# Optimization experiments

Measured on AMD Instinct MI355X. Metric: run time of the kernel, lower is better.

Reference implementation:

```python
import jax, jax.numpy as jnp
import numpy as np

STEPS = 10
HIDDEN = 16


def _lift_world(uv, depth, cam2world, intrinsics):
    # uv: [B,N,2], depth: [B,N], returns world coords [B,N,3]
    fx = intrinsics[:, 0, 0][:, None]
    fy = intrinsics[:, 1, 1][:, None]
    cx = intrinsics[:, 0, 2][:, None]
    cy = intrinsics[:, 1, 2][:, None]
    x_lift = (uv[:, :, 0] - cx) / fx * depth
    y_lift = (uv[:, :, 1] - cy) / fy * depth
    pts_hom = jnp.stack((x_lift, y_lift, depth, jnp.ones_like(depth)), axis=-1)  # [B,N,4]
    world = jnp.einsum('bij,bnj->bni', cam2world, pts_hom)[:, :, :3]
    return world


def reference(cam2world, intrinsics, uv, initial_depth,
              W_phi, b_phi, W_ih, b_ih, W_hh, b_hh, W_out, b_out):
    B, N, _ = uv.shape
    F = W_phi.shape[1]

    # ray directions through pixels (z_cam = 1 plane)
    pixel_pts = _lift_world(uv, jnp.ones((B, N), uv.dtype), cam2world, intrinsics)
    cam_pos = cam2world[:, :3, 3]
    ray_dirs = pixel_pts - cam_pos[:, None, :]
    ray_dirs = ray_dirs / jnp.linalg.norm(ray_dirs, axis=2, keepdims=True)

    world0 = _lift_world(uv, initial_depth[:, :, 0], cam2world, intrinsics)

    h0 = jnp.zeros((B * N, HIDDEN), world0.dtype)
    c0 = jnp.zeros((B * N, HIDDEN), world0.dtype)

    def step(carry, _):
        world, h, c = carry
        # phi: per-point feature net (stand-in: relu(Linear 3->F))
        v = jax.nn.relu(jnp.einsum('bnd,df->bnf', world, W_phi) + b_phi)
        x = v.reshape(B * N, F)
        gates = x @ W_ih.T + b_ih + h @ W_hh.T + b_hh  # [BN, 4H]
        i, f, g, o = jnp.split(gates, 4, axis=1)  # torch LSTMCell gate order
        c = jax.nn.sigmoid(f) * c + jax.nn.sigmoid(i) * jnp.tanh(g)
        h = jax.nn.sigmoid(o) * jnp.tanh(c)
        sd = (h @ W_out.T + b_out).reshape(B, N, 1)  # signed distance
        world = world + ray_dirs * sd
        return (world, h, c), None

    (world, _, _), _ = jax.lax.scan(step, (world0, h0, c0), None, length=STEPS)

    # final depth: camera-frame z of world points
    pts_hom = jnp.concatenate((world, jnp.ones((B, N, 1), world.dtype)), axis=2)
    c2w_inv = jnp.linalg.inv(cam2world)
    pts_cam = jnp.einsum('bij,bnj->bni', c2w_inv, pts_hom)
    depth = pts_cam[:, :, 2:3]
    return world, depth


def setup_inputs() -> dict:
    key = jax.random.key(0)
    ks = jax.random.split(key, 12)
    B, N, F = 8, 16384, 256
    H = HIDDEN

    # cam2world: proper-ish poses (orthonormal rotation via QR + translation)
    R = jnp.linalg.qr(jax.random.normal(ks[0], (B, 3, 3)))[0]
    t = jax.random.normal(ks[1], (B, 3)) * 2.0
    cam2world = jnp.zeros((B, 4, 4)).at[:, :3, :3].set(R).at[:, :3, 3].set(t).at[:, 3, 3].set(1.0)

    intrinsics = jnp.zeros((B, 3, 3))
    intrinsics = intrinsics.at[:, 0, 0].set(500.0).at[:, 1, 1].set(500.0)
    intrinsics = intrinsics.at[:, 0, 2].set(64.0).at[:, 1, 2].set(64.0).at[:, 2, 2].set(1.0)

    uv = jax.random.uniform(ks[2], (B, N, 2)) * 128.0  # pixel coords in a 128x128 image
    initial_depth = 0.05 + 0.0005 * jax.random.normal(ks[3], (B, N, 1))

    s = 1.0 / np.sqrt(F)
    return {
        'cam2world': cam2world.astype(jnp.float32),
        'intrinsics': intrinsics.astype(jnp.float32),
        'uv': uv.astype(jnp.float32),
        'initial_depth': initial_depth.astype(jnp.float32),
        'W_phi': jax.random.normal(ks[4], (3, F)) * 0.5,
        'b_phi': jax.random.normal(ks[5], (F,)) * 0.01,
        'W_ih': jax.random.normal(ks[6], (4 * H, F)) * s,
        'b_ih': jnp.zeros((4 * H,)).at[H:2 * H].set(1.0),  # forget-gate bias init
        'W_hh': jnp.linalg.qr(jax.random.normal(ks[7], (4 * H, H)))[0][:4 * H],
        'b_hh': jnp.zeros((4 * H,)),
        'W_out': jax.random.normal(ks[8], (1, H)) * (1.0 / np.sqrt(H)),
        'b_out': jnp.zeros((1,)),
    }
```

## Files before the change

### kernel.cpp

```cpp
#include <hip/hip_runtime.h>
#include <math.h>

#define FEAT 256
#define HID  16
#define STEPS 10

#define AW_N    16384
#define PHI_OFF 16384
#define PHI_N   4096
#define WHA_OFF 20480
#define WHA_N   1024
#define TOT_N   21504

typedef unsigned short ushort_t;
typedef __attribute__((ext_vector_type(8)))  short  short8;
typedef __attribute__((ext_vector_type(16))) float  floatx16;
typedef __attribute__((ext_vector_type(4)))  unsigned int uintx4;

__device__ __forceinline__ ushort_t f2bf_bits(float f) {
    union { float f; unsigned u; } cv; cv.f = f;
    unsigned u = cv.u;
    u = (u + 0x7FFFu + ((u >> 16) & 1u)) >> 16;
    return (ushort_t)u;
}

__device__ __forceinline__ unsigned pk2bf(float lo, float hi) {
    unsigned r;
    asm("v_cvt_pk_bf16_f32 %0, %1, %2" : "=v"(r) : "v"(lo), "v"(hi));
    return r;
}

__device__ __forceinline__ unsigned relupk(float a, float b) {
    return pk2bf(fmaxf(a, 0.f), fmaxf(b, 0.f));
}

__device__ __forceinline__ unsigned packhl(float x) {
    unsigned u = __float_as_uint(x);
    float hi = __uint_as_float(u & 0xFFFF0000u);
    return pk2bf(hi, x - hi);
}

__device__ __forceinline__ void plswap(unsigned &a, unsigned &b) {
#if __has_builtin(__builtin_amdgcn_permlane32_swap)
    auto r = __builtin_amdgcn_permlane32_swap(a, b, false, false);
    a = (unsigned)r[0]; b = (unsigned)r[1];
#else
    unsigned xa = (unsigned)__shfl_xor((int)a, 32, 64);
    unsigned xb = (unsigned)__shfl_xor((int)b, 32, 64);
    bool hi = (threadIdx.x & 63) >= 32;
    unsigned na = hi ? xb : a;
    unsigned nb = hi ? b : xa;
    a = na; b = nb;
#endif
}

__device__ __forceinline__ short8 mk8(unsigned a, unsigned b, unsigned c, unsigned d) {
    union { unsigned u[4]; short8 s; } cv;
    cv.u[0] = a; cv.u[1] = b; cv.u[2] = c; cv.u[3] = d;
    return cv.s;
}

__global__ void prep(const float* __restrict__ Wphi, const float* __restrict__ bphi,
                     const float* __restrict__ Wih,  const float* __restrict__ Whh,
                     void* __restrict__ ws) {
    int idx = blockIdx.x * 256 + threadIdx.x;
    const float L = 1.4426950408889634f;
    ushort_t* p = (ushort_t*)ws;
    if (idx < AW_N) {
        int e    = idx & 7;
        int lane = (idx >> 3) & 63;
        int kt   = (idx >> 9) & 1;
        int gt   = (idx >> 10) & 1;
        int kc   = idx >> 11;
        int gate = gt * 32 + (lane & 31);
        int feat = kc * 32 + kt * 16 + (lane >> 5) * 8 + e;
        float sc = (gate >= 32 && gate < 48) ? (2.f * L) : L;
        p[idx] = f2bf_bits(Wih[gate * FEAT + feat] * sc);
    } else if (idx < WHA_OFF) {
        int j    = idx - PHI_OFF;
        int e    = j & 7;
        int lane = (j >> 3) & 63;
        int ft   = j >> 9;
        float v = 0.f;
        if (lane < 32) {
            int f = ft * 32 + (lane & 31);
            if (e < 6)       v = Wphi[(e >> 1) * FEAT + f];
            else if (e == 6) v = bphi[f];
        }
        p[idx] = f2bf_bits(v);
    } else if (idx < TOT_N) {
        int j    = idx - WHA_OFF;
        int e    = j & 7;
        int lane = (j >> 3) & 63;
        int gt   = j >> 9;
        int gate = gt * 32 + (lane & 31);
        int k    = (lane >> 5) * 8 + e;
        float sc = (gate >= 32 && gate < 48) ? (2.f * L) : L;
        p[idx] = f2bf_bits(Whh[gate * HID + k] * sc);
    }
}

__global__ __launch_bounds__(256, 2) void march(
    const float* __restrict__ c2w, const float* __restrict__ intr,
    const float* __restrict__ uv,  const float* __restrict__ dep0,
    const void* __restrict__ ws,
    const float* __restrict__ bih, const float* __restrict__ bhh,
    const float* __restrict__ Wout, const float* __restrict__ bout,
    float* __restrict__ out, int B, int N) {

    __shared__ __align__(16) ushort_t Slds[AW_N + PHI_N];

    int tid = threadIdx.x;
    int l = tid & 63;
    int l31 = l & 31;
    bool hi32 = (l >= 32);
    int ray = blockIdx.x * 256 + tid;
    int BN = B * N;
    int b = ray / N;

    const float L = 1.4426950408889634f;

    {
        const uintx4* src = (const uintx4*)ws;
        uintx4* dst = (uintx4*)Slds;
        for (int i = tid; i < (AW_N + PHI_N) / 8; i += 256) dst[i] = src[i];
    }
    const short8* aw8 = (const short8*)Slds;

    short8 whA0, whA1;
    {
        const short8* wha = (const short8*)((const ushort_t*)ws + WHA_OFF);
        whA0 = wha[l];
        whA1 = wha[64 + l];
    }

    float wjv[8];
#pragma unroll
    for (int q = 0; q < 8; ++q) wjv[q] = Wout[(q & 3) + 4 * (int)hi32 + 8 * (q >> 2)];
    float bo = bout[0];

    floatx16 gb0, gb1;
#pragma unroll
    for (int r = 0; r < 16; ++r) {
        int loc = (r & 3) + 8 * (r >> 2) + 4 * (int)hi32;
        gb0[r] = L * (bih[loc] + bhh[loc]);
        float sc1 = (r < 8) ? (2.f * L) : L;
        gb1[r] = sc1 * (bih[32 + loc] + bhh[32 + loc]);
    }

    const float* M = c2w + b * 16;
    float R00 = M[0], R01 = M[1], R02 = M[2], t0 = M[3];
    float R10 = M[4], R11 = M[5], R12 = M[6], t1 = M[7];
    float R20 = M[8], R21 = M[9], R22 = M[10], t2 = M[11];
    const float* Kc = intr + b * 9;
    float fx = Kc[0], cx = Kc[2], fy = Kc[4], cy = Kc[5];

    float u = uv[ray * 2 + 0];
    float v = uv[ray * 2 + 1];
    float d0 = dep0[ray];

    float xl = (u - cx) / fx;
    float yl = (v - cy) / fy;
    float dx = R00 * xl + R01 * yl + R02;
    float dy = R10 * xl + R11 * yl + R12;
    float dz = R20 * xl + R21 * yl + R22;
    float invn = rsqrtf(dx * dx + dy * dy + dz * dz);
    float rdx = dx * invn, rdy = dy * invn, rdz = dz * invn;
    float w0 = fmaf(dx, d0, t0);
    float w1 = fmaf(dy, d0, t1);
    float w2 = fmaf(dz, d0, t2);

    short8 z8 = {0, 0, 0, 0, 0, 0, 0, 0};
    short8 hB0 = z8, hB1 = z8;

    float cst[16];
#pragma unroll
    for (int j = 0; j < 16; ++j) cst[j] = 0.f;

    __syncthreads();

#pragma unroll 1
    for (int s = 0; s < STEPS; ++s) {
        float s0 = __shfl(w0, l31 + 32);
        float s1 = __shfl(w1, l31 + 32);
        float s2 = __shfl(w2, l31 + 32);
        short8 bw0, bw1;
        {
            unsigned a0 = hi32 ? 0u : packhl(w0);
            unsigned a1 = hi32 ? 0u : packhl(w1);
            unsigned a2 = hi32 ? 0u : packhl(w2);
            unsigned a3 = hi32 ? 0u : 0x00003F80u;
            unsigned c0 = hi32 ? 0u : packhl(s0);
            unsigned c1 = hi32 ? 0u : packhl(s1);
            unsigned c2 = hi32 ? 0u : packhl(s2);
            bw0 = mk8(a0, a1, a2, a3);
            bw1 = mk8(c0, c1, c2, a3);
        }

        floatx16 a00 = gb0, a01 = gb0;
        floatx16 a10 = gb1, a11 = gb1;

        floatx16 zz = (floatx16){0.f,0.f,0.f,0.f,0.f,0.f,0.f,0.f,
                                 0.f,0.f,0.f,0.f,0.f,0.f,0.f,0.f};

#pragma unroll
        for (int kc = 0; kc < 8; ++kc) {
            short8 aphi = aw8[(AW_N / 8) + kc * 64 + l];
            floatx16 p0 = __builtin_amdgcn_mfma_f32_32x32x16_bf16(aphi, bw0, zz, 0, 0, 0);
            floatx16 p1 = __builtin_amdgcn_mfma_f32_32x32x16_bf16(aphi, bw1, zz, 0, 0, 0);

            unsigned P0[8], P1[8];
#pragma unroll
            for (int q = 0; q < 8; ++q) {
                P0[q] = relupk(p0[2 * q], p0[2 * q + 1]);
                P1[q] = relupk(p1[2 * q], p1[2 * q + 1]);
            }
            plswap(P0[0], P0[2]); plswap(P0[1], P0[3]);
            plswap(P0[4], P0[6]); plswap(P0[5], P0[7]);
            plswap(P1[0], P1[2]); plswap(P1[1], P1[3]);
            plswap(P1[4], P1[6]); plswap(P1[5], P1[7]);
            short8 b00 = mk8(P0[0], P0[1], P0[2], P0[3]);
            short8 b01 = mk8(P0[4], P0[5], P0[6], P0[7]);
            short8 b10 = mk8(P1[0], P1[1], P1[2], P1[3]);
            short8 b11 = mk8(P1[4], P1[5], P1[6], P1[7]);

            short8 wA00 = aw8[(kc * 4 + 0) * 64 + l];
            short8 wA01 = aw8[(kc * 4 + 1) * 64 + l];
            short8 wA10 = aw8[(kc * 4 + 2) * 64 + l];
            short8 wA11 = aw8[(kc * 4 + 3) * 64 + l];

            a00 = __builtin_amdgcn_mfma_f32_32x32x16_bf16(wA00, b00, a00, 0, 0, 0);
            a00 = __builtin_amdgcn_mfma_f32_32x32x16_bf16(wA01, b01, a00, 0, 0, 0);
            a10 = __builtin_amdgcn_mfma_f32_32x32x16_bf16(wA10, b00, a10, 0, 0, 0);
            a10 = __builtin_amdgcn_mfma_f32_32x32x16_bf16(wA11, b01, a10, 0, 0, 0);
            a01 = __builtin_amdgcn_mfma_f32_32x32x16_bf16(wA00, b10, a01, 0, 0, 0);
            a01 = __builtin_amdgcn_mfma_f32_32x32x16_bf16(wA01, b11, a01, 0, 0, 0);
            a11 = __builtin_amdgcn_mfma_f32_32x32x16_bf16(wA10, b10, a11, 0, 0, 0);
            a11 = __builtin_amdgcn_mfma_f32_32x32x16_bf16(wA11, b11, a11, 0, 0, 0);
        }

        a00 = __builtin_amdgcn_mfma_f32_32x32x16_bf16(whA0, hB0, a00, 0, 0, 0);
        a10 = __builtin_amdgcn_mfma_f32_32x32x16_bf16(whA1, hB0, a10, 0, 0, 0);
        a01 = __builtin_amdgcn_mfma_f32_32x32x16_bf16(whA0, hB1, a01, 0, 0, 0);
        a11 = __builtin_amdgcn_mfma_f32_32x32x16_bf16(whA1, hB1, a11, 0, 0, 0);

        const float L2 = 2.8853900817779268f;
        float h0[8], h1[8];
#pragma unroll
        for (int q = 0; q < 8; ++q) {
            {
                float ig = __builtin_amdgcn_rcpf(1.f + __builtin_amdgcn_exp2f(-a00[q]));
                float fg = __builtin_amdgcn_rcpf(1.f + __builtin_amdgcn_exp2f(-a00[8 + q]));
                float gg = fmaf(-2.f, __builtin_amdgcn_rcpf(1.f + __builtin_amdgcn_exp2f(a10[q])), 1.f);
                float og = __builtin_amdgcn_rcpf(1.f + __builtin_amdgcn_exp2f(-a10[8 + q]));
                float cn = fmaf(fg, cst[q], ig * gg);
                cst[q] = cn;
                float tc = fmaf(-2.f, __builtin_amdgcn_rcpf(1.f + __builtin_amdgcn_exp2f(L2 * cn)), 1.f);
                h0[q] = og * tc;
            }
            {
                float ig = __builtin_amdgcn_rcpf(1.f + __builtin_amdgcn_exp2f(-a01[q]));
                float fg = __builtin_amdgcn_rcpf(1.f + __builtin_amdgcn_exp2f(-a01[8 + q]));
                float gg = fmaf(-2.f, __builtin_amdgcn_rcpf(1.f + __builtin_amdgcn_exp2f(a11[q])), 1.f);
                float og = __builtin_amdgcn_rcpf(1.f + __builtin_amdgcn_exp2f(-a11[8 + q]));
                float cn = fmaf(fg, cst[8 + q], ig * gg);
                cst[8 + q] = cn;
                float tc = fmaf(-2.f, __builtin_amdgcn_rcpf(1.f + __builtin_amdgcn_exp2f(L2 * cn)), 1.f);
                h1[q] = og * tc;
            }
        }

        float sd0 = 0.f, sd1 = 0.f;
#pragma unroll
        for (int q = 0; q < 8; ++q) {
            sd0 = fmaf(h0[q], wjv[q], sd0);
            sd1 = fmaf(h1[q], wjv[q], sd1);
        }
        sd0 += __shfl_xor(sd0, 32, 64);
        sd1 += __shfl_xor(sd1, 32, 64);
        float sdv = (hi32 ? sd1 : sd0) + bo;

        {
            unsigned QA = pk2bf(h0[0], h0[1]), QB = pk2bf(h0[2], h0[3]);
            unsigned QC = pk2bf(h0[4], h0[5]), QD = pk2bf(h0[6], h0[7]);
            plswap(QA, QC); plswap(QB, QD);
            hB0 = mk8(QA, QB, QC, QD);
            unsigned RA = pk2bf(h1[0], h1[1]), RB = pk2bf(h1[2], h1[3]);
            unsigned RC = pk2bf(h1[4], h1[5]), RD = pk2bf(h1[6], h1[7]);
            plswap(RA, RC); plswap(RB, RD);
            hB1 = mk8(RA, RB, RC, RD);
        }

        w0 = fmaf(rdx, sdv, w0);
        w1 = fmaf(rdy, sdv, w1);
        w2 = fmaf(rdz, sdv, w2);
    }

    int base = ray * 3;
    out[base + 0] = w0;
    out[base + 1] = w1;
    out[base + 2] = w2;
    float dd = R02 * (w0 - t0) + R12 * (w1 - t1) + R22 * (w2 - t2);
    out[BN * 3 + ray] = dd;
}

extern "C" void kernel_launch(void* const* d_in, const int* in_sizes, int n_in,
                              void* d_out, int out_size, void* d_ws, size_t ws_size,
                              hipStream_t stream) {
    const float* c2w  = (const float*)d_in[0];
    const float* intr = (const float*)d_in[1];
    const float* uv   = (const float*)d_in[2];
    const float* dep  = (const float*)d_in[3];
    const float* Wphi = (const float*)d_in[4];
    const float* bphi = (const float*)d_in[5];
    const float* Wih  = (const float*)d_in[6];
    const float* bih  = (const float*)d_in[7];
    const float* Whh  = (const float*)d_in[8];
    const float* bhh  = (const float*)d_in[9];
    const float* Wout = (const float*)d_in[10];
    const float* bout = (const float*)d_in[11];
    float* out = (float*)d_out;

    int B = in_sizes[0] / 16;
    int BN = in_sizes[3];
    int N = BN / B;
    int blocks = (BN + 255) / 256;

    prep<<<(TOT_N + 255) / 256, 256, 0, stream>>>(Wphi, bphi, Wih, Whh, d_ws);
    march<<<blocks, 256, 0, stream>>>(c2w, intr, uv, dep, d_ws,
                                      bih, bhh, Wout, bout, out, B, N);
}
```

Measured before the change: 141.4 us.

## Process 32 rays per wave instead of 64 to raise occupancy

Each wave now handles one 32-ray MFMA column tile instead of two, which halves the accumulators, cell state and hidden registers. Launch bounds go from 2 to 4 blocks per CU. The phi weights are now read from global memory instead of LDS, which shrinks the shared allocation. The cost is twice the blocks and half the MFMA work per wave, so the Wih weights in LDS get less reuse per load, and the upper half-wave duplicates work and skips the store.

Result: slower. 152.3 us (+7.6%).

```diff
diff --git a/kernel.cpp b/kernel.cpp
--- a/kernel.cpp
+++ b/kernel.cpp
@@ -100,7 +100,7 @@
     }
 }
 
-__global__ __launch_bounds__(256, 2) void march(
+__global__ __launch_bounds__(256, 4) void march(
     const float* __restrict__ c2w, const float* __restrict__ intr,
     const float* __restrict__ uv,  const float* __restrict__ dep0,
     const void* __restrict__ ws,
@@ -108,13 +108,13 @@
     const float* __restrict__ Wout, const float* __restrict__ bout,
     float* __restrict__ out, int B, int N) {
 
-    __shared__ __align__(16) ushort_t Slds[AW_N + PHI_N];
+    __shared__ __align__(16) ushort_t Slds[AW_N];
 
     int tid = threadIdx.x;
-    int l = tid & 63;
+    int wv = tid >> 6, l = tid & 63;
     int l31 = l & 31;
     bool hi32 = (l >= 32);
-    int ray = blockIdx.x * 256 + tid;
+    int ray = blockIdx.x * 128 + wv * 32 + l31;
     int BN = B * N;
     int b = ray / N;
 
@@ -123,9 +123,10 @@
     {
         const uintx4* src = (const uintx4*)ws;
         uintx4* dst = (uintx4*)Slds;
-        for (int i = tid; i < (AW_N + PHI_N) / 8; i += 256) dst[i] = src[i];
+        for (int i = tid; i < AW_N / 8; i += 256) dst[i] = src[i];
     }
     const short8* aw8 = (const short8*)Slds;
+    const short8* phi8 = (const short8*)((const ushort_t*)ws + PHI_OFF);
 
     short8 whA0, whA1;
     {
@@ -171,124 +172,82 @@
     float w2 = fmaf(dz, d0, t2);
 
     short8 z8 = {0, 0, 0, 0, 0, 0, 0, 0};
-    short8 hB0 = z8, hB1 = z8;
-
-    float cst[16];
-#pragma unroll
-    for (int j = 0; j < 16; ++j) cst[j] = 0.f;
+    short8 hB = z8;
+
+    float cst[8];
+#pragma unroll
+    for (int j = 0; j < 8; ++j) cst[j] = 0.f;
 
     __syncthreads();
 
 #pragma unroll 1
     for (int s = 0; s < STEPS; ++s) {
-        float s0 = __shfl(w0, l31 + 32);
-        float s1 = __shfl(w1, l31 + 32);
-        float s2 = __shfl(w2, l31 + 32);
-        short8 bw0, bw1;
+        short8 bw;
         {
             unsigned a0 = hi32 ? 0u : packhl(w0);
             unsigned a1 = hi32 ? 0u : packhl(w1);
             unsigned a2 = hi32 ? 0u : packhl(w2);
             unsigned a3 = hi32 ? 0u : 0x00003F80u;
-            unsigned c0 = hi32 ? 0u : packhl(s0);
-            unsigned c1 = hi32 ? 0u : packhl(s1);
-            unsigned c2 = hi32 ? 0u : packhl(s2);
-            bw0 = mk8(a0, a1, a2, a3);
-            bw1 = mk8(c0, c1, c2, a3);
-        }
-
-        floatx16 a00 = gb0, a01 = gb0;
-        floatx16 a10 = gb1, a11 = gb1;
-
+            bw = mk8(a0, a1, a2, a3);
+        }
+
+        floatx16 a0 = gb0, a1 = gb1;
         floatx16 zz = (floatx16){0.f,0.f,0.f,0.f,0.f,0.f,0.f,0.f,
                                  0.f,0.f,0.f,0.f,0.f,0.f,0.f,0.f};
 
 #pragma unroll
         for (int kc = 0; kc < 8; ++kc) {
-            short8 aphi = aw8[(AW_N / 8) + kc * 64 + l];
-            floatx16 p0 = __builtin_amdgcn_mfma_f32_32x32x16_bf16(aphi, bw0, zz, 0, 0, 0);
-            floatx16 p1 = __builtin_amdgcn_mfma_f32_32x32x16_bf16(aphi, bw1, zz, 0, 0, 0);
-
-            unsigned P0[8], P1[8];
-#pragma unroll
-            for (int q = 0; q < 8; ++q) {
-                P0[q] = relupk(p0[2 * q], p0[2 * q + 1]);
-                P1[q] = relupk(p1[2 * q], p1[2 * q + 1]);
-            }
-            plswap(P0[0], P0[2]); plswap(P0[1], P0[3]);
-            plswap(P0[4], P0[6]); plswap(P0[5], P0[7]);
-            plswap(P1[0], P1[2]); plswap(P1[1], P1[3]);
-            plswap(P1[4], P1[6]); plswap(P1[5], P1[7]);
-            short8 b00 = mk8(P0[0], P0[1], P0[2], P0[3]);
-            short8 b01 = mk8(P0[4], P0[5], P0[6], P0[7]);
-            short8 b10 = mk8(P1[0], P1[1], P1[2], P1[3]);
-            short8 b11 = mk8(P1[4], P1[5], P1[6], P1[7]);
+            short8 aphi = phi8[kc * 64 + l];
+            floatx16 p = __builtin_amdgcn_mfma_f32_32x32x16_bf16(aphi, bw, zz, 0, 0, 0);
+
+            unsigned P[8];
+#pragma unroll
+            for (int q = 0; q < 8; ++q)
+                P[q] = relupk(p[2 * q], p[2 * q + 1]);
+            plswap(P[0], P[2]); plswap(P[1], P[3]);
+            plswap(P[4], P[6]); plswap(P[5], P[7]);
+            short8 b0 = mk8(P[0], P[1], P[2], P[3]);
+            short8 b1 = mk8(P[4], P[5], P[6], P[7]);
 
             short8 wA00 = aw8[(kc * 4 + 0) * 64 + l];
             short8 wA01 = aw8[(kc * 4 + 1) * 64 + l];
             short8 wA10 = aw8[(kc * 4 + 2) * 64 + l];
             short8 wA11 = aw8[(kc * 4 + 3) * 64 + l];
 
-            a00 = __builtin_amdgcn_mfma_f32_32x32x16_bf16(wA00, b00, a00, 0, 0, 0);
-            a00 = __builtin_amdgcn_mfma_f32_32x32x16_bf16(wA01, b01, a00, 0, 0, 0);
-            a10 = __builtin_amdgcn_mfma_f32_32x32x16_bf16(wA10, b00, a10, 0, 0, 0);
-            a10 = __builtin_amdgcn_mfma_f32_32x32x16_bf16(wA11, b01, a10, 0, 0, 0);
-            a01 = __builtin_amdgcn_mfma_f32_32x32x16_bf16(wA00, b10, a01, 0, 0, 0);
-            a01 = __builtin_amdgcn_mfma_f32_32x32x16_bf16(wA01, b11, a01, 0, 0, 0);
-            a11 = __builtin_amdgcn_mfma_f32_32x32x16_bf16(wA10, b10, a11, 0, 0, 0);
-            a11 = __builtin_amdgcn_mfma_f32_32x32x16_bf16(wA11, b11, a11, 0, 0, 0);
-        }
-
-        a00 = __builtin_amdgcn_mfma_f32_32x32x16_bf16(whA0, hB0, a00, 0, 0, 0);
-        a10 = __builtin_amdgcn_mfma_f32_32x32x16_bf16(whA1, hB0, a10, 0, 0, 0);
-        a01 = __builtin_amdgcn_mfma_f32_32x32x16_bf16(whA0, hB1, a01, 0, 0, 0);
-        a11 = __builtin_amdgcn_mfma_f32_32x32x16_bf16(whA1, hB1, a11, 0, 0, 0);
+            a0 = __builtin_amdgcn_mfma_f32_32x32x16_bf16(wA00, b0, a0, 0, 0, 0);
+            a0 = __builtin_amdgcn_mfma_f32_32x32x16_bf16(wA01, b1, a0, 0, 0, 0);
+            a1 = __builtin_amdgcn_mfma_f32_32x32x16_bf16(wA10, b0, a1, 0, 0, 0);
+            a1 = __builtin_amdgcn_mfma_f32_32x32x16_bf16(wA11, b1, a1, 0, 0, 0);
+        }
+
+        a0 = __builtin_amdgcn_mfma_f32_32x32x16_bf16(whA0, hB, a0, 0, 0, 0);
+        a1 = __builtin_amdgcn_mfma_f32_32x32x16_bf16(whA1, hB, a1, 0, 0, 0);
 
         const float L2 = 2.8853900817779268f;
-        float h0[8], h1[8];
+        float h0[8];
 #pragma unroll
         for (int q = 0; q < 8; ++q) {
-            {
-                float ig = __builtin_amdgcn_rcpf(1.f + __builtin_amdgcn_exp2f(-a00[q]));
-                float fg = __builtin_amdgcn_rcpf(1.f + __builtin_amdgcn_exp2f(-a00[8 + q]));
-                float gg = fmaf(-2.f, __builtin_amdgcn_rcpf(1.f + __builtin_amdgcn_exp2f(a10[q])), 1.f);
-                float og = __builtin_amdgcn_rcpf(1.f + __builtin_amdgcn_exp2f(-a10[8 + q]));
-                float cn = fmaf(fg, cst[q], ig * gg);
-                cst[q] = cn;
-                float tc = fmaf(-2.f, __builtin_amdgcn_rcpf(1.f + __builtin_amdgcn_exp2f(L2 * cn)), 1.f);
-                h0[q] = og * tc;
-            }
-            {
-                float ig = __builtin_amdgcn_rcpf(1.f + __builtin_amdgcn_exp2f(-a01[q]));
-                float fg = __builtin_amdgcn_rcpf(1.f + __builtin_amdgcn_exp2f(-a01[8 + q]));
-                float gg = fmaf(-2.f, __builtin_amdgcn_rcpf(1.f + __builtin_amdgcn_exp2f(a11[q])), 1.f);
-                float og = __builtin_amdgcn_rcpf(1.f + __builtin_amdgcn_exp2f(-a11[8 + q]));
-                float cn = fmaf(fg, cst[8 + q], ig * gg);
-                cst[8 + q] = cn;
-                float tc = fmaf(-2.f, __builtin_amdgcn_rcpf(1.f + __builtin_amdgcn_exp2f(L2 * cn)), 1.f);
-                h1[q] = og * tc;
-            }
-        }
-
-        float sd0 = 0.f, sd1 = 0.f;
-#pragma unroll
-        for (int q = 0; q < 8; ++q) {
-            sd0 = fmaf(h0[q], wjv[q], sd0);
-            sd1 = fmaf(h1[q], wjv[q], sd1);
-        }
-        sd0 += __shfl_xor(sd0, 32, 64);
-        sd1 += __shfl_xor(sd1, 32, 64);
-        float sdv = (hi32 ? sd1 : sd0) + bo;
+            float ig = __builtin_amdgcn_rcpf(1.f + __builtin_amdgcn_exp2f(-a0[q]));
+            float fg = __builtin_amdgcn_rcpf(1.f + __builtin_amdgcn_exp2f(-a0[8 + q]));
+            float gg = fmaf(-2.f, __builtin_amdgcn_rcpf(1.f + __builtin_amdgcn_exp2f(a1[q])), 1.f);
+            float og = __builtin_amdgcn_rcpf(1.f + __builtin_amdgcn_exp2f(-a1[8 + q]));
+            float cn = fmaf(fg, cst[q], ig * gg);
+            cst[q] = cn;
+            float tc = fmaf(-2.f, __builtin_amdgcn_rcpf(1.f + __builtin_amdgcn_exp2f(L2 * cn)), 1.f);
+            h0[q] = og * tc;
+        }
+
+        float sd = 0.f;
+#pragma unroll
+        for (int q = 0; q < 8; ++q) sd = fmaf(h0[q], wjv[q], sd);
+        sd += __shfl_xor(sd, 32, 64);
+        float sdv = sd + bo;
 
         {
             unsigned QA = pk2bf(h0[0], h0[1]), QB = pk2bf(h0[2], h0[3]);
             unsigned QC = pk2bf(h0[4], h0[5]), QD = pk2bf(h0[6], h0[7]);
             plswap(QA, QC); plswap(QB, QD);
-            hB0 = mk8(QA, QB, QC, QD);
-            unsigned RA = pk2bf(h1[0], h1[1]), RB = pk2bf(h1[2], h1[3]);
-            unsigned RC = pk2bf(h1[4], h1[5]), RD = pk2bf(h1[6], h1[7]);
-            plswap(RA, RC); plswap(RB, RD);
-            hB1 = mk8(RA, RB, RC, RD);
+            hB = mk8(QA, QB, QC, QD);
         }
 
         w0 = fmaf(rdx, sdv, w0);
@@ -296,12 +255,14 @@
         w2 = fmaf(rdz, sdv, w2);
     }
 
-    int base = ray * 3;
-    out[base + 0] = w0;
-    out[base + 1] = w1;
-    out[base + 2] = w2;
-    float dd = R02 * (w0 - t0) + R12 * (w1 - t1) + R22 * (w2 - t2);
-    out[BN * 3 + ray] = dd;
+    if (!hi32) {
+        int base = ray * 3;
+        out[base + 0] = w0;
+        out[base + 1] = w1;
+        out[base + 2] = w2;
+        float dd = R02 * (w0 - t0) + R12 * (w1 - t1) + R22 * (w2 - t2);
+        out[BN * 3 + ray] = dd;
+    }
 }
 
 extern "C" void kernel_launch(void* const* d_in, const int* in_sizes, int n_in,
@@ -324,7 +285,7 @@
     int B = in_sizes[0] / 16;
     int BN = in_sizes[3];
     int N = BN / B;
-    int blocks = (BN + 255) / 256;
+    int blocks = (BN + 127) / 128;
 
     prep<<<(TOT_N + 255) / 256, 256, 0, stream>>>(Wphi, bphi, Wih, Whh, d_ws);
     march<<<blocks, 256, 0, stream>>>(c2w, intr, uv, dep, d_ws,
```
